# Performance work log

Hardware: AMD Instinct MI355X
Metric: run time of the kernel (lower is better)

The kernel has to match this reference:

```python
import jax, jax.numpy as jnp
import numpy as np

N, LQ, C, M, L, P = 8, 2048, 256, 8, 4, 4
DH = C // M  # 32
LENS = (2048, 1024, 512, 256)


def setup_inputs() -> dict:
    key = jax.random.key(0)
    ks = jax.random.split(key, 8)
    s = 1.0 / np.sqrt(C)
    return {
        "query": jax.random.normal(ks[0], (N, LQ, C), jnp.float32),
        "reference_points": jax.random.uniform(ks[1], (N, LQ, L, 1), jnp.float32),
        "input_flatten": jax.random.normal(ks[2], (N, sum(LENS), C), jnp.float32),
        "temporal_lens": np.array(LENS, np.int64),
        "level_start_index": np.array([0, 2048, 3072, 3584], np.int64),
        "W_off": jax.random.normal(ks[3], (C, M * L * P), jnp.float32) * 0.01,
        "b_off": jax.random.normal(ks[4], (M * L * P,), jnp.float32),
        "W_attn": jax.random.normal(ks[5], (C, M * L * P), jnp.float32) * 0.01,
        "b_attn": jnp.zeros((M * L * P,), jnp.float32),
        "W_val": jax.random.normal(ks[6], (C, C), jnp.float32) * s,
        "b_val": jnp.zeros((C,), jnp.float32),
        "W_out": jax.random.normal(ks[7], (C, C), jnp.float32) * s,
        "b_out": jnp.zeros((C,), jnp.float32),
    }


def _deform_core(value, lens, loc, attn):
    # value: (N, S, M, DH); loc, attn: (N, LQ, M, L, P); loc in normalized [0,1] coords.
    # Equivalent to per-level F.grid_sample (bilinear, zeros padding, align_corners=False)
    # on a 1xT image: pixel position = loc*T - 0.5; the y-coord 0.5 lands exactly on row 0.
    outs = []
    start = 0
    for l, T in enumerate(lens):
        v = value[:, start:start + T].transpose(0, 2, 1, 3)  # (N, M, T, DH)
        start += T
        pos = loc[..., l, :] * T - 0.5                       # (N, LQ, M, P)
        x0f = jnp.floor(pos)
        frac = pos - x0f
        x0 = x0f.astype(jnp.int32)

        def gather(idx):
            i = jnp.clip(idx, 0, T - 1).transpose(0, 2, 1, 3).reshape(N, M, LQ * P, 1)
            return jnp.take_along_axis(v, i, axis=2).reshape(N, M, LQ, P, DH)

        in0 = ((x0 >= 0) & (x0 < T)).astype(value.dtype)
        in1 = ((x0 + 1 >= 0) & (x0 + 1 < T)).astype(value.dtype)
        w0 = ((1.0 - frac) * in0).transpose(0, 2, 1, 3)[..., None]  # (N, M, LQ, P, 1)
        w1 = (frac * in1).transpose(0, 2, 1, 3)[..., None]
        outs.append(gather(x0) * w0 + gather(x0 + 1) * w1)          # (N, M, LQ, P, DH)
    sampled = jnp.stack(outs, axis=3)          # (N, M, LQ, L, P, DH)
    aw = attn.transpose(0, 2, 1, 3, 4)         # (N, M, LQ, L, P)
    return jnp.einsum('nmqlpd,nmqlp->nqmd', sampled, aw).reshape(N, LQ, C)


def reference(query, reference_points, input_flatten, temporal_lens, level_start_index,
              W_off, b_off, W_attn, b_attn, W_val, b_val, W_out, b_out):
    lens = [int(t) for t in np.asarray(temporal_lens)[:L]]  # static per-level lengths
    value = (input_flatten @ W_val + b_val).reshape(N, -1, M, DH)
    off = (query @ W_off + b_off).reshape(N, LQ, M, L, P)
    attn = jax.nn.softmax((query @ W_attn + b_attn).reshape(N, LQ, M, L * P), axis=-1)
    attn = attn.reshape(N, LQ, M, L, P)
    norm = jnp.asarray(lens, query.dtype)                    # offset_normalizer (L,)
    loc = reference_points[:, :, None, :, None, 0] + off / norm[None, None, None, :, None]
    out = _deform_core(value, lens, loc, attn)
    out = out @ W_out + b_out
    return out, loc, attn
```

## Files before the change

kernel.cpp:

```cpp
#include <hip/hip_runtime.h>
#include <hip/hip_bf16.h>
#include <math.h>

#define NB 8
#define LQ 2048
#define SSUM 3840

typedef unsigned short ushort_t;
typedef unsigned int uint_t;
typedef __attribute__((ext_vector_type(8))) short bf16x8;
typedef __attribute__((ext_vector_type(4))) float f32x4;

__device__ __forceinline__ ushort_t f2bf(float f) {
  __hip_bfloat16 h = __float2bfloat16(f);
  return *reinterpret_cast<ushort_t*>(&h);
}
__device__ __forceinline__ uint_t pk2bf(float lo, float hi) {
  float2 t; t.x = lo; t.y = hi;
  __hip_bfloat162 h = __float22bfloat162_rn(t);
  return *reinterpret_cast<uint_t*>(&h);
}
__device__ __forceinline__ float bf2f_lo(uint_t u) {
  union { uint_t u32; float f; } x;
  x.u32 = u << 16;
  return x.f;
}
__device__ __forceinline__ float bf2f_hi(uint_t u) {
  union { uint_t u32; float f; } x;
  x.u32 = u & 0xffff0000u;
  return x.f;
}
__device__ __forceinline__ void ld_lds16(const void* g, void* l) {
  __builtin_amdgcn_global_load_lds(
      (const __attribute__((address_space(1))) void*)g,
      (__attribute__((address_space(3))) void*)l, 16, 0, 0);
}

__global__ __launch_bounds__(256) void prep(
    const float* __restrict__ W_val, const float* __restrict__ W_off,
    const float* __restrict__ W_attn, const float* __restrict__ W_out,
    ushort_t* __restrict__ BtVal, ushort_t* __restrict__ BtOA,
    ushort_t* __restrict__ BtOut) {
  const int b = blockIdx.x, t = threadIdx.x;
  if (b < 256) { BtVal[b * 256 + t] = f2bf(W_val[(size_t)t * 256 + b]); return; }
  if (b < 512) { int n = b - 256; BtOut[n * 256 + t] = f2bf(W_out[(size_t)t * 256 + n]); return; }
  if (b < 640) { int n = b - 512; BtOA[n * 256 + t] = f2bf(W_off[(size_t)t * 128 + n]); return; }
  int n = b - 640; BtOA[(128 + n) * 256 + t] = f2bf(W_attn[(size_t)t * 128 + n]);
}

template <bool AF32>
__global__ __launch_bounds__(256) void gemm_fused(
    int job_base,
    const float* __restrict__ in_flat, const float* __restrict__ query,
    const ushort_t* core,
    const ushort_t* __restrict__ BtVal, const ushort_t* __restrict__ BtOA,
    const ushort_t* __restrict__ BtOut,
    const float* __restrict__ b_val, const float* __restrict__ b_off,
    const float* __restrict__ b_attn, const float* __restrict__ b_out,
    ushort_t* value, float* __restrict__ loc,
    float* __restrict__ attn, float* __restrict__ out) {
  __shared__ ushort_t Ab[3][64][32];
  __shared__ ushort_t Bb[3][256][32];

  const int job = job_base + blockIdx.x;

  const float* Afp = nullptr;
  const ushort_t* Abf = nullptr;
  const ushort_t* Bt;
  const float* bias_lo; const float* bias_hi;
  int bm, cstride;
  ushort_t* Cb = nullptr;
  float* Cf_lo = nullptr; float* Cf_hi = nullptr;

  if (job < 480) {
    bm = job * 64; Afp = in_flat; Bt = BtVal;
    bias_lo = b_val; bias_hi = b_val + 128; Cb = value; cstride = 256;
  } else if (job < 736) {
    bm = (job - 480) * 64; Afp = query; Bt = BtOA;
    bias_lo = b_off; bias_hi = b_attn; Cf_lo = loc; Cf_hi = attn; cstride = 128;
  } else {
    bm = (job - 736) * 64; Abf = core; Bt = BtOut;
    bias_lo = b_out; bias_hi = b_out + 128; Cf_lo = out; Cf_hi = out + 128;
    cstride = 256;
  }

  const int tid = threadIdx.x;
  const int lane = tid & 63;
  const int wv = tid >> 6;
  const int quad = lane >> 4;
  const int l16 = lane & 15;
  const int wm = (wv >> 1) * 32;
  const int wn = (wv & 1) * 128;
  const int drow = lane >> 2;
  const int dk = (lane & 3) * 8;

  f32x4 acc[2][8];
#pragma unroll
  for (int i = 0; i < 2; ++i)
#pragma unroll
    for (int j = 0; j < 8; ++j) acc[i][j] = (f32x4)(0.f);

  auto stageB = [&](int sb, int k0) {
#pragma unroll
    for (int c = 0; c < 4; ++c)
      ld_lds16(Bt + (size_t)(wv * 64 + c * 16 + drow) * 256 + k0 + dk,
               &Bb[sb][wv * 64 + c * 16 + drow][dk]);
  };
  auto stageA_dma = [&](int sb, int k0) {
    ld_lds16(Abf + (size_t)(bm + wv * 16 + drow) * 256 + k0 + dk,
             &Ab[sb][wv * 16 + drow][dk]);
  };
  float4 ra[2][2];
  auto issueA = [&](int ph, int k0) {
    const float* gp = Afp + (size_t)(bm + wv * 16 + drow) * 256 + k0 + dk;
    ra[ph][0] = *(const float4*)gp;
    ra[ph][1] = *(const float4*)(gp + 4);
  };
  auto writeA = [&](int ph, int sb) {
    uint4 c;
    c.x = pk2bf(ra[ph][0].x, ra[ph][0].y);
    c.y = pk2bf(ra[ph][0].z, ra[ph][0].w);
    c.z = pk2bf(ra[ph][1].x, ra[ph][1].y);
    c.w = pk2bf(ra[ph][1].z, ra[ph][1].w);
    *(uint4*)&Ab[sb][wv * 16 + drow][dk] = c;
  };

  if (AF32) {
    issueA(0, 0);   stageB(0, 0);
    issueA(1, 32);  stageB(1, 32);
    writeA(0, 0);
  } else {
    stageA_dma(0, 0);  stageB(0, 0);
    stageA_dma(1, 32); stageB(1, 32);
  }

#pragma unroll
  for (int it = 0; it < 8; ++it) {
    if (it < 7) {
      if (AF32) asm volatile("s_waitcnt vmcnt(4)" ::: "memory");
      else      asm volatile("s_waitcnt vmcnt(5)" ::: "memory");
    } else {
      asm volatile("s_waitcnt vmcnt(0)" ::: "memory");
    }
    asm volatile("s_waitcnt lgkmcnt(0)" ::: "memory");
    __builtin_amdgcn_s_barrier();
    __builtin_amdgcn_sched_barrier(0);

    if (it < 6) {
      if (AF32) issueA(it & 1, (it + 2) * 32);
      else      stageA_dma((it + 2) % 3, (it + 2) * 32);
      stageB((it + 2) % 3, (it + 2) * 32);
    }
    if (AF32 && it < 7)
      writeA((it ^ 1) & 1, (it + 1) % 3);

    const int sb = it % 3;
    bf16x8 af[2], bfr[8];
#pragma unroll
    for (int mi = 0; mi < 2; ++mi)
      af[mi] = *(const bf16x8*)&Ab[sb][wm + mi * 16 + l16][quad * 8];
#pragma unroll
    for (int ni = 0; ni < 8; ++ni)
      bfr[ni] = *(const bf16x8*)&Bb[sb][wn + ni * 16 + l16][quad * 8];
#pragma unroll
    for (int mi = 0; mi < 2; ++mi)
#pragma unroll
      for (int ni = 0; ni < 8; ++ni)
        acc[mi][ni] = __builtin_amdgcn_mfma_f32_16x16x32_bf16(af[mi], bfr[ni], acc[mi][ni], 0, 0, 0);
  }

  const int hi = wv & 1;
  const float* bias = hi ? bias_hi : bias_lo;
  ushort_t* Cbw = Cb ? (Cb + (hi ? 128 : 0)) : nullptr;
  float* Cfw = hi ? Cf_hi : Cf_lo;

#pragma unroll
  for (int ni = 0; ni < 8; ++ni) {
    int cc = ni * 16 + l16;
    float bv = bias[cc];
#pragma unroll
    for (int mi = 0; mi < 2; ++mi) {
      f32x4 v = acc[mi][ni];
      int rbase = bm + wm + mi * 16 + quad * 4;
#pragma unroll
      for (int r = 0; r < 4; ++r) {
        float o = v[r] + bv;
        size_t idx = (size_t)(rbase + r) * cstride + cc;
        if (Cbw) Cbw[idx] = f2bf(o);
        else     Cfw[idx] = o;
      }
    }
  }
}

__global__ __launch_bounds__(256) void deform_fused(
    const ushort_t* __restrict__ value,
    float* __restrict__ locbuf,
    float* __restrict__ attnbuf,
    const float* __restrict__ refp,
    ushort_t* __restrict__ core) {
  const int tid = threadIdx.x;
  const int bid = blockIdx.x;
  const int swz = (bid & 7) * 512 + (bid >> 3);
  const int nq0 = swz * 4;
  const int n = nq0 >> 11;

  __shared__ float4 sp[512];

#pragma unroll
  for (int j = 0; j < 2; ++j) {
    int s = tid + j * 256;
    int q = s >> 7;
    int r = s & 127;
    int m = r >> 4;
    int lp = r & 15;
    int l = lp >> 2;
    int T = 2048 >> l;
    int start = 4096 - (4096 >> l);
    float rn = (float)(1 << l) * (1.0f / 2048.0f);

    float lraw = locbuf[(size_t)nq0 * 128 + s];
    float logit = attnbuf[(size_t)nq0 * 128 + s];
    float lv = refp[(size_t)(nq0 + q) * 4 + l] + lraw * rn;
    locbuf[(size_t)nq0 * 128 + s] = lv;

    float mx = logit;
    mx = fmaxf(mx, __shfl_xor(mx, 1, 64));
    mx = fmaxf(mx, __shfl_xor(mx, 2, 64));
    mx = fmaxf(mx, __shfl_xor(mx, 4, 64));
    mx = fmaxf(mx, __shfl_xor(mx, 8, 64));
    float e = __expf(logit - mx);
    float sm = e;
    sm += __shfl_xor(sm, 1, 64);
    sm += __shfl_xor(sm, 2, 64);
    sm += __shfl_xor(sm, 4, 64);
    sm += __shfl_xor(sm, 8, 64);
    float aw = e / sm;
    attnbuf[(size_t)nq0 * 128 + s] = aw;

    float pos = lv * (float)T - 0.5f;
    float x0f = floorf(pos);
    float fr = pos - x0f;
    int x0 = (int)x0f;
    float w0 = ((unsigned)x0 < (unsigned)T) ? (1.f - fr) * aw : 0.f;
    float w1 = ((unsigned)(x0 + 1) < (unsigned)T) ? fr * aw : 0.f;
    int i0 = min(max(x0, 0), T - 1);
    int i1 = min(max(x0 + 1, 0), T - 1);
    float4 pr;
    pr.x = w0;
    pr.y = w1;
    pr.z = __int_as_float((start + i0) * 256);
    pr.w = __int_as_float((start + i1) * 256);
    sp[q * 128 + lp * 8 + m] = pr;
  }
  __syncthreads();

  const int q = tid >> 6;
  const int t64 = tid & 63;
  const int m = t64 >> 3;
  const int g = t64 & 7;
  const ushort_t* vbase = value + (size_t)n * (SSUM * 256) + m * 32 + g * 4;

  float a0 = 0.f, a1 = 0.f, a2 = 0.f, a3 = 0.f;
#pragma unroll
  for (int lp = 0; lp < 16; ++lp) {
    float4 pr = sp[q * 128 + lp * 8 + m];
    int o0 = __float_as_int(pr.z);
    int o1 = __float_as_int(pr.w);
    uint2 u0 = *(const uint2*)(vbase + o0);
    uint2 u1 = *(const uint2*)(vbase + o1);
    a0 += pr.x * bf2f_lo(u0.x) + pr.y * bf2f_lo(u1.x);
    a1 += pr.x * bf2f_hi(u0.x) + pr.y * bf2f_hi(u1.x);
    a2 += pr.x * bf2f_lo(u0.y) + pr.y * bf2f_lo(u1.y);
    a3 += pr.x * bf2f_hi(u0.y) + pr.y * bf2f_hi(u1.y);
  }
  uint2 outp;
  outp.x = (uint_t)f2bf(a0) | ((uint_t)f2bf(a1) << 16);
  outp.y = (uint_t)f2bf(a2) | ((uint_t)f2bf(a3) << 16);
  *(uint2*)&core[(size_t)(nq0 + q) * 256 + m * 32 + g * 4] = outp;
}

extern "C" void kernel_launch(void* const* d_in, const int* in_sizes, int n_in,
                              void* d_out, int out_size, void* d_ws, size_t ws_size,
                              hipStream_t stream) {
  const float* query    = (const float*)d_in[0];
  const float* refpts   = (const float*)d_in[1];
  const float* in_flat  = (const float*)d_in[2];
  const float* W_off  = (const float*)d_in[5];
  const float* b_off  = (const float*)d_in[6];
  const float* W_attn = (const float*)d_in[7];
  const float* b_attn = (const float*)d_in[8];
  const float* W_val  = (const float*)d_in[9];
  const float* b_val  = (const float*)d_in[10];
  const float* W_out  = (const float*)d_in[11];
  const float* b_out  = (const float*)d_in[12];

  float* out  = (float*)d_out;
  float* loc  = out + (size_t)NB * LQ * 256;
  float* attn = loc + (size_t)NB * LQ * 128;

  ushort_t* value = (ushort_t*)d_ws;
  ushort_t* core  = value + (size_t)NB * SSUM * 256;
  ushort_t* BtVal = core + (size_t)NB * LQ * 256;
  ushort_t* BtOA  = BtVal + 65536;
  ushort_t* BtOut = BtOA + 65536;

  const int Mq = NB * LQ;

  prep<<<768, 256, 0, stream>>>(W_val, W_off, W_attn, W_out, BtVal, BtOA, BtOut);

  gemm_fused<true><<<736, 256, 0, stream>>>(
      0, in_flat, query, core, BtVal, BtOA, BtOut,
      b_val, b_off, b_attn, b_out, value, loc, attn, out);

  deform_fused<<<Mq / 4, 256, 0, stream>>>(value, loc, attn, refpts, core);

  gemm_fused<false><<<256, 256, 0, stream>>>(
      736, in_flat, query, core, BtVal, BtOA, BtOut,
      b_val, b_off, b_attn, b_out, value, loc, attn, out);
}
```

Before: 167.4 us.

## Halve output GEMM tile width, double-buffer B stage, and restructure prefetch

The output-projection GEMM now uses 128-wide N tiles, launching 512 blocks instead of 256 to fill more CUs. The B-tile LDS buffer drops from triple to double buffering with a one-step-ahead prefetch, which shrinks shared memory and raises occupancy. The A-fragment LDS reads are moved ahead of the f32-to-bf16 A write, and the waitcnt thresholds are retuned to match. The shallower B prefetch may expose more global load latency per iteration.

New measurement: 158.3 us. -5.4%, faster.

```diff
diff --git a/kernel.cpp b/kernel.cpp
--- a/kernel.cpp
+++ b/kernel.cpp
@@ -48,9 +48,8 @@
   int n = b - 640; BtOA[(128 + n) * 256 + t] = f2bf(W_attn[(size_t)t * 128 + n]);
 }
 
-template <bool AF32>
+template <bool AF32, int BN>
 __global__ __launch_bounds__(256) void gemm_fused(
-    int job_base,
     const float* __restrict__ in_flat, const float* __restrict__ query,
     const ushort_t* core,
     const ushort_t* __restrict__ BtVal, const ushort_t* __restrict__ BtOA,
@@ -59,10 +58,10 @@
     const float* __restrict__ b_attn, const float* __restrict__ b_out,
     ushort_t* value, float* __restrict__ loc,
     float* __restrict__ attn, float* __restrict__ out) {
+  constexpr int NFR = BN / 32;
+  constexpr int BC  = BN / 64;
   __shared__ ushort_t Ab[3][64][32];
-  __shared__ ushort_t Bb[3][256][32];
-
-  const int job = job_base + blockIdx.x;
+  __shared__ ushort_t Bb[2][BN][32];
 
   const float* Afp = nullptr;
   const ushort_t* Abf = nullptr;
@@ -72,16 +71,22 @@
   ushort_t* Cb = nullptr;
   float* Cf_lo = nullptr; float* Cf_hi = nullptr;
 
-  if (job < 480) {
-    bm = job * 64; Afp = in_flat; Bt = BtVal;
-    bias_lo = b_val; bias_hi = b_val + 128; Cb = value; cstride = 256;
-  } else if (job < 736) {
-    bm = (job - 480) * 64; Afp = query; Bt = BtOA;
-    bias_lo = b_off; bias_hi = b_attn; Cf_lo = loc; Cf_hi = attn; cstride = 128;
+  if (AF32) {
+    const int job = blockIdx.x;
+    if (job < 480) {
+      bm = job * 64; Afp = in_flat; Bt = BtVal;
+      bias_lo = b_val; bias_hi = b_val + 128; Cb = value; cstride = 256;
+    } else {
+      bm = (job - 480) * 64; Afp = query; Bt = BtOA;
+      bias_lo = b_off; bias_hi = b_attn; Cf_lo = loc; Cf_hi = attn; cstride = 128;
+    }
   } else {
-    bm = (job - 736) * 64; Abf = core; Bt = BtOut;
-    bias_lo = b_out; bias_hi = b_out + 128; Cf_lo = out; Cf_hi = out + 128;
-    cstride = 256;
+    const int jb = blockIdx.x;
+    bm = (jb >> 1) * 64;
+    const int nb = (jb & 1) * 128;
+    Abf = core; Bt = BtOut + nb * 256;
+    bias_lo = b_out + nb; bias_hi = b_out + nb + 64;
+    Cf_lo = out + nb; Cf_hi = out + nb + 64; cstride = 256;
   }
 
   const int tid = threadIdx.x;
@@ -90,21 +95,21 @@
   const int quad = lane >> 4;
   const int l16 = lane & 15;
   const int wm = (wv >> 1) * 32;
-  const int wn = (wv & 1) * 128;
+  const int wn = (wv & 1) * (BN / 2);
   const int drow = lane >> 2;
   const int dk = (lane & 3) * 8;
 
-  f32x4 acc[2][8];
+  f32x4 acc[2][NFR];
 #pragma unroll
   for (int i = 0; i < 2; ++i)
 #pragma unroll
-    for (int j = 0; j < 8; ++j) acc[i][j] = (f32x4)(0.f);
-
-  auto stageB = [&](int sb, int k0) {
-#pragma unroll
-    for (int c = 0; c < 4; ++c)
-      ld_lds16(Bt + (size_t)(wv * 64 + c * 16 + drow) * 256 + k0 + dk,
-               &Bb[sb][wv * 64 + c * 16 + drow][dk]);
+    for (int j = 0; j < NFR; ++j) acc[i][j] = (f32x4)(0.f);
+
+  auto stageB = [&](int db, int k0) {
+#pragma unroll
+    for (int c = 0; c < BC; ++c)
+      ld_lds16(Bt + (size_t)(wv * (BN / 4) + c * 16 + drow) * 256 + k0 + dk,
+               &Bb[db][wv * (BN / 4) + c * 16 + drow][dk]);
   };
   auto stageA_dma = [&](int sb, int k0) {
     ld_lds16(Abf + (size_t)(bm + wv * 16 + drow) * 256 + k0 + dk,
@@ -126,19 +131,21 @@
   };
 
   if (AF32) {
-    issueA(0, 0);   stageB(0, 0);
-    issueA(1, 32);  stageB(1, 32);
+    issueA(0, 0);
+    stageB(0, 0);
+    issueA(1, 32);
     writeA(0, 0);
   } else {
-    stageA_dma(0, 0);  stageB(0, 0);
-    stageA_dma(1, 32); stageB(1, 32);
+    stageA_dma(0, 0);
+    stageB(0, 0);
+    stageA_dma(1, 32);
   }
 
 #pragma unroll
   for (int it = 0; it < 8; ++it) {
     if (it < 7) {
-      if (AF32) asm volatile("s_waitcnt vmcnt(4)" ::: "memory");
-      else      asm volatile("s_waitcnt vmcnt(5)" ::: "memory");
+      if (AF32) asm volatile("s_waitcnt vmcnt(2)" ::: "memory");
+      else      asm volatile("s_waitcnt vmcnt(1)" ::: "memory");
     } else {
       asm volatile("s_waitcnt vmcnt(0)" ::: "memory");
     }
@@ -146,26 +153,30 @@
     __builtin_amdgcn_s_barrier();
     __builtin_amdgcn_sched_barrier(0);
 
-    if (it < 6) {
-      if (AF32) issueA(it & 1, (it + 2) * 32);
-      else      stageA_dma((it + 2) % 3, (it + 2) * 32);
-      stageB((it + 2) % 3, (it + 2) * 32);
+    if (it < 7) stageB((it + 1) & 1, (it + 1) * 32);
+    if (AF32) {
+      if (it < 6) issueA(it & 1, (it + 2) * 32);
+    } else {
+      if (it < 6) stageA_dma((it + 2) % 3, (it + 2) * 32);
     }
+
+    const int sb = it % 3;
+    const int bb = it & 1;
+    bf16x8 af[2], bfr[NFR];
+#pragma unroll
+    for (int mi = 0; mi < 2; ++mi)
+      af[mi] = *(const bf16x8*)&Ab[AF32 ? (it % 3) : sb][wm + mi * 16 + l16][quad * 8];
+#pragma unroll
+    for (int ni = 0; ni < NFR; ++ni)
+      bfr[ni] = *(const bf16x8*)&Bb[bb][wn + ni * 16 + l16][quad * 8];
+
     if (AF32 && it < 7)
       writeA((it ^ 1) & 1, (it + 1) % 3);
 
-    const int sb = it % 3;
-    bf16x8 af[2], bfr[8];
 #pragma unroll
     for (int mi = 0; mi < 2; ++mi)
-      af[mi] = *(const bf16x8*)&Ab[sb][wm + mi * 16 + l16][quad * 8];
-#pragma unroll
-    for (int ni = 0; ni < 8; ++ni)
-      bfr[ni] = *(const bf16x8*)&Bb[sb][wn + ni * 16 + l16][quad * 8];
-#pragma unroll
-    for (int mi = 0; mi < 2; ++mi)
-#pragma unroll
-      for (int ni = 0; ni < 8; ++ni)
+#pragma unroll
+      for (int ni = 0; ni < NFR; ++ni)
         acc[mi][ni] = __builtin_amdgcn_mfma_f32_16x16x32_bf16(af[mi], bfr[ni], acc[mi][ni], 0, 0, 0);
   }
 
@@ -175,7 +186,7 @@
   float* Cfw = hi ? Cf_hi : Cf_lo;
 
 #pragma unroll
-  for (int ni = 0; ni < 8; ++ni) {
+  for (int ni = 0; ni < NFR; ++ni) {
     int cc = ni * 16 + l16;
     float bv = bias[cc];
 #pragma unroll
@@ -309,13 +320,13 @@
 
   prep<<<768, 256, 0, stream>>>(W_val, W_off, W_attn, W_out, BtVal, BtOA, BtOut);
 
-  gemm_fused<true><<<736, 256, 0, stream>>>(
-      0, in_flat, query, core, BtVal, BtOA, BtOut,
+  gemm_fused<true, 256><<<736, 256, 0, stream>>>(
+      in_flat, query, core, BtVal, BtOA, BtOut,
       b_val, b_off, b_attn, b_out, value, loc, attn, out);
 
   deform_fused<<<Mq / 4, 256, 0, stream>>>(value, loc, attn, refpts, core);
 
-  gemm_fused<false><<<256, 256, 0, stream>>>(
-      736, in_flat, query, core, BtVal, BtOA, BtOut,
+  gemm_fused<false, 128><<<512, 256, 0, stream>>>(
+      in_flat, query, core, BtVal, BtOA, BtOut,
       b_val, b_off, b_attn, b_out, value, loc, attn, out);
 }
```
